# Optimization experiments

Hardware: AMD Instinct MI355X
Metric: run time of the kernel (lower is better)

Reference implementation:

```python
import jax, jax.numpy as jnp
import numpy as np

N, MAX_NB, H, L, V, B, M = 16384, 15, 512, 128, 1024, 256, 65536


def setup_inputs() -> dict:
    key = jax.random.key(0)
    ks = jax.random.split(key, 32)
    s = 0.02  # param init scale
    inp = {
        'x_ids': jax.random.randint(ks[0], (N,), 0, V, dtype=jnp.int32),
        'contexts': jax.random.randint(ks[1], (N,), 0, B, dtype=jnp.int32),
        'nei_idx': jax.random.randint(ks[2], (N, MAX_NB), 0, M, dtype=jnp.int32),
        'nei_mask': jax.random.randint(ks[3], (N, MAX_NB), 0, 2, dtype=jnp.int32),
        'o_idx': jax.random.randint(ks[4], (N, MAX_NB), 0, M, dtype=jnp.int32),
        'o_mask': jax.random.randint(ks[5], (N, MAX_NB), 0, 2, dtype=jnp.int32),
        'H_msg': jax.random.normal(ks[6], (M, H), jnp.float32),
        'x_tree_vecs': jax.random.normal(ks[7], (B, L), jnp.float32),
        'embedding': jax.random.normal(ks[8], (V, H), jnp.float32) * s,
        'Wz_w': jax.random.normal(ks[9], (H, 2 * H), jnp.float32) * s,
        'Wz_b': jnp.zeros((H,), jnp.float32),
        'Wr_w': jax.random.normal(ks[10], (H, H), jnp.float32) * s,
        'Wr_b': jnp.zeros((H,), jnp.float32),
        'Ur_w': jax.random.normal(ks[11], (H, H), jnp.float32) * s,
        'Wh_w': jax.random.normal(ks[12], (H, 2 * H), jnp.float32) * s,
        'Wh_b': jnp.zeros((H,), jnp.float32),
        'W_w': jax.random.normal(ks[13], (H, H + L), jnp.float32) * s,
        'W_b': jnp.zeros((H,), jnp.float32),
        'Wo_w': jax.random.normal(ks[14], (V, H), jnp.float32) * s,
        'Wo_b': jnp.zeros((V,), jnp.float32),
        'Ui_w': jax.random.normal(ks[15], (H, 2 * H), jnp.float32) * s,
        'Ui_b': jnp.zeros((H,), jnp.float32),
        'U_w': jax.random.normal(ks[16], (H, H + L), jnp.float32) * s,
        'U_b': jnp.zeros((H,), jnp.float32),
        'Uo_w': jax.random.normal(ks[17], (1, H), jnp.float32) * s,
        'Uo_b': jnp.zeros((1,), jnp.float32),
    }
    return inp


def _gru(x, h_nei, Wz_w, Wz_b, Wr_w, Wr_b, Ur_w, Wh_w, Wh_b):
    # x: [N,H], h_nei: [N,MAX_NB,H]
    sum_h = h_nei.sum(axis=1)
    z = jax.nn.sigmoid(jnp.concatenate([x, sum_h], axis=1) @ Wz_w.T + Wz_b)
    r1 = (x @ Wr_w.T + Wr_b)[:, None, :]          # [N,1,H]
    r2 = jnp.einsum('nkh,gh->nkg', h_nei, Ur_w)   # U_r(h_nei), no bias
    r = jax.nn.sigmoid(r1 + r2)
    sum_gated = (r * h_nei).sum(axis=1)
    pre_h = jnp.tanh(jnp.concatenate([x, sum_gated], axis=1) @ Wh_w.T + Wh_b)
    return (1.0 - z) * sum_h + z * pre_h


def reference(x_ids, contexts, nei_idx, nei_mask, o_idx, o_mask, H_msg,
              x_tree_vecs, embedding, Wz_w, Wz_b, Wr_w, Wr_b, Ur_w,
              Wh_w, Wh_b, W_w, W_b, Wo_w, Wo_b, Ui_w, Ui_b, U_w, U_b,
              Uo_w, Uo_b):
    x = embedding[x_ids]                                   # [N,H]
    h_nei = H_msg[nei_idx] * nei_mask[..., None].astype(H_msg.dtype)  # [N,NB,H]
    o_nei = H_msg[o_idx] * o_mask[..., None].astype(H_msg.dtype)
    new_h = _gru(x, h_nei, Wz_w, Wz_b, Wr_w, Wr_b, Ur_w, Wh_w, Wh_b)
    cur_o = o_nei.sum(axis=1)                              # [N,H]
    ctx = x_tree_vecs[contexts]                            # [N,L]
    # word prediction: aggregate(new_h, contexts, x_tree_vecs, 'word')
    w_hid = jax.nn.relu(jnp.concatenate([new_h, ctx], axis=1) @ W_w.T + W_b)
    word_scores = w_hid @ Wo_w.T + Wo_b                    # [N,V]
    # stop prediction: U_i(cat(x, cur_o)) -> aggregate(..., 'stop')
    stop_h = jax.nn.relu(jnp.concatenate([x, cur_o], axis=1) @ Ui_w.T + Ui_b)
    s_hid = jax.nn.relu(jnp.concatenate([stop_h, ctx], axis=1) @ U_w.T + U_b)
    stop_scores = s_hid @ Uo_w.T + Uo_b                    # [N,1]
    return jnp.concatenate([word_scores, stop_scores], axis=1)  # [N,V+1]
```

## Files before the change

### kernel.cpp

```cpp
#include <hip/hip_runtime.h>
#include <hip/hip_bf16.h>

typedef unsigned short u16;
typedef unsigned int u32;
typedef __attribute__((ext_vector_type(8))) short s8v;
typedef __attribute__((ext_vector_type(4))) float f4v;

#define HDIM 512
#define NNODE 16384
#define NB 15

__device__ __forceinline__ u16 f2bu(float x) {
  union { float f; u32 i; } v; v.f = x;
  u32 r = v.i + 0x7FFFu + ((v.i >> 16) & 1u);
  return (u16)(r >> 16);
}
__device__ __forceinline__ float bu2f(u16 u) {
  union { u32 i; float f; } v; v.i = ((u32)u) << 16;
  return v.f;
}
__device__ __forceinline__ u32 pk(float a, float b) {
  return (u32)f2bu(a) | ((u32)f2bu(b) << 16);
}
__device__ __forceinline__ float sigm(float x) {
  return __builtin_amdgcn_rcpf(1.f + __expf(-x));
}
__device__ __forceinline__ void gl16(const void* g, void* l) {
  __builtin_amdgcn_global_load_lds(
      (const __attribute__((address_space(1))) u32*)g,
      (__attribute__((address_space(3))) u32*)l, 16, 0, 0);
}
template<int N> __device__ __forceinline__ void wait_vm() {
  if constexpr (N == 0) asm volatile("s_waitcnt vmcnt(0)" ::: "memory");
  else if constexpr (N == 2) asm volatile("s_waitcnt vmcnt(2)" ::: "memory");
  else asm volatile("s_waitcnt vmcnt(4)" ::: "memory");
}

__global__ __launch_bounds__(256) void k_cvt_all(
    const float* Wz_w, const float* Wr_w, const float* Wh_w, const float* Ui_w,
    const float* Ur_w, const float* W_w, const float* U_w, const float* Wo_w,
    const float* emb, const float* xtree,
    const float* Wz_b, const float* Wr_b, const float* Wh_b, const float* Ui_b,
    const float* W_b, const float* U_b,
    u16* wcat, u16* wz_h, u16* wh_h, u16* ui_h, u16* ur, u16* w_n, u16* u_n,
    u16* ccat, u16* wo, u16* emb_bf, u16* xt_bf, float* ebias, float* cbias) {
  int seg = blockIdx.y;
  const float* src = nullptr; u16* dst = nullptr;
  const float* fsrc = nullptr; float* fdst = nullptr;
  int R = 0, Cs = 0, c0 = 0, C = 0, fn = 0;
  switch (seg) {
    case 0:  src = Wz_w; dst = wcat;              R = 512;  Cs = 1024; c0 = 0;   C = 512; break;
    case 1:  src = Wr_w; dst = wcat + 512 * 512;  R = 512;  Cs = 512;  c0 = 0;   C = 512; break;
    case 2:  src = Wh_w; dst = wcat + 1024 * 512; R = 512;  Cs = 1024; c0 = 0;   C = 512; break;
    case 3:  src = Ui_w; dst = wcat + 1536 * 512; R = 512;  Cs = 1024; c0 = 0;   C = 512; break;
    case 4:  src = Wz_w; dst = wz_h;              R = 512;  Cs = 1024; c0 = 512; C = 512; break;
    case 5:  src = Wh_w; dst = wh_h;              R = 512;  Cs = 1024; c0 = 512; C = 512; break;
    case 6:  src = Ui_w; dst = ui_h;              R = 512;  Cs = 1024; c0 = 512; C = 512; break;
    case 7:  src = Ur_w; dst = ur;                R = 512;  Cs = 512;  c0 = 0;   C = 512; break;
    case 8:  src = W_w;  dst = w_n;               R = 512;  Cs = 640;  c0 = 0;   C = 512; break;
    case 9:  src = U_w;  dst = u_n;               R = 512;  Cs = 640;  c0 = 0;   C = 512; break;
    case 10: src = W_w;  dst = ccat;              R = 512;  Cs = 640;  c0 = 512; C = 128; break;
    case 11: src = U_w;  dst = ccat + 512 * 128;  R = 512;  Cs = 640;  c0 = 512; C = 128; break;
    case 12: src = Wo_w; dst = wo;                R = 1024; Cs = 512;  c0 = 0;   C = 512; break;
    case 13: src = emb;  dst = emb_bf;            R = 1024; Cs = 512;  c0 = 0;   C = 512; break;
    case 14: src = xtree; dst = xt_bf;            R = 256;  Cs = 128;  c0 = 0;   C = 128; break;
    case 15: fsrc = Wz_b; fdst = ebias;        fn = 512; break;
    case 16: fsrc = Wr_b; fdst = ebias + 512;  fn = 512; break;
    case 17: fsrc = Wh_b; fdst = ebias + 1024; fn = 512; break;
    case 18: fsrc = Ui_b; fdst = ebias + 1536; fn = 512; break;
    case 19: fsrc = W_b;  fdst = cbias;        fn = 512; break;
    case 20: fsrc = U_b;  fdst = cbias + 512;  fn = 512; break;
  }
  int i = blockIdx.x * 256 + threadIdx.x;
  if (fdst) { if (i < fn) fdst[i] = fsrc[i]; return; }
  int e0 = i * 8;
  if (e0 >= R * C) return;
  int r = e0 / C, c = e0 - r * C;
  const float* s = src + (size_t)r * Cs + c0 + c;
  float4 a = *reinterpret_cast<const float4*>(s);
  float4 b = *reinterpret_cast<const float4*>(s + 4);
  uint4 o = {pk(a.x, a.y), pk(a.z, a.w), pk(b.x, b.y), pk(b.z, b.w)};
  *reinterpret_cast<uint4*>(&dst[e0]) = o;
}

struct GP {
  const u16* A; const u16* B; int K; int lda;
  const float* gadd; int ldg; const int* gidx;
  const float* bias; const u16* shb;
  float* outf; u16* outh; int ldo;
};

template<int EP>
__device__ __forceinline__ void epi(int row, int col, float v, const GP& g) {
  if constexpr (EP == 0) {
    g.outf[(size_t)row * g.ldo + col] = v + (g.bias ? g.bias[col] : 0.f);
  } else if constexpr (EP == 3) {
    float pre = v + g.gadd[(size_t)g.gidx[row] * g.ldg + col];
    g.outh[(size_t)row * g.ldo + col] = f2bu(pre > 0.f ? pre : 0.f);
  } else {
    g.outh[(size_t)row * g.ldo + col] = f2bu(v);
  }
}

__device__ __forceinline__ void swz_tile(int nx, int ny, int& m0, int& n0) {
  int orig = blockIdx.y * nx + blockIdx.x;
  int q = (nx * ny) >> 3;
  int tile = (orig & 7) * q + (orig >> 3);
  n0 = (tile % nx) * 128;
  m0 = (tile / nx) * 128;
}

template<int EP, int KV>
__device__ void gemm_core(const GP& g, u16* AsB, u16* BsB, int m0, int n0) {
  const int tid = threadIdx.x, lane = tid & 63, w = tid >> 6;
  const int wm = (w >> 2) * 64, wn = (w & 3) * 32;

  const int sr = tid >> 2, sc = (tid & 3) ^ ((sr >> 1) & 3);
  const u16* gA = g.A + (size_t)(m0 + sr) * g.lda + sc * 8;
  const u16* gB = g.B + (size_t)(n0 + sr) * KV + sc * 8;
  const int ls = tid * 8;

  f4v acc[4][2];
  f4v z4 = {0.f, 0.f, 0.f, 0.f};
#pragma unroll
  for (int a = 0; a < 4; a++) { acc[a][0] = z4; acc[a][1] = z4; }

  constexpr int T = KV / 32;
  auto STAGE = [&](int t) {
    int buf = (t & 3) * 4096;
    gl16(gA + t * 32, AsB + buf + ls);
    gl16(gB + t * 32, BsB + buf + ls);
  };
  STAGE(0); STAGE(1); STAGE(2);

#pragma unroll
  for (int t = 0; t < T; t++) {
    if (t < T - 2) wait_vm<4>();
    else if (t == T - 2) wait_vm<2>();
    else wait_vm<0>();
    __builtin_amdgcn_s_barrier();
    asm volatile("" ::: "memory");
    if (t + 3 < T) STAGE(t + 3);
    const u16* as = AsB + (t & 3) * 4096;
    const u16* bs = BsB + (t & 3) * 4096;
    s8v af[4], bf[2];
    int cc = lane >> 4;
#pragma unroll
    for (int i = 0; i < 4; i++) {
      int R = wm + i * 16 + (lane & 15);
      af[i] = *reinterpret_cast<const s8v*>(
          &as[R * 32 + (cc ^ ((R >> 1) & 3)) * 8]);
    }
#pragma unroll
    for (int i = 0; i < 2; i++) {
      int C = wn + i * 16 + (lane & 15);
      bf[i] = *reinterpret_cast<const s8v*>(
          &bs[C * 32 + (cc ^ ((C >> 1) & 3)) * 8]);
    }
    __builtin_amdgcn_s_setprio(1);
#pragma unroll
    for (int mi = 0; mi < 4; mi++)
#pragma unroll
      for (int ni = 0; ni < 2; ni++)
        acc[mi][ni] = __builtin_amdgcn_mfma_f32_16x16x32_bf16(
            af[mi], bf[ni], acc[mi][ni], 0, 0, 0);
    __builtin_amdgcn_s_setprio(0);
  }
#pragma unroll
  for (int mi = 0; mi < 4; mi++)
#pragma unroll
    for (int ni = 0; ni < 2; ni++)
#pragma unroll
      for (int r = 0; r < 4; r++) {
        int row = m0 + wm + mi * 16 + (lane >> 4) * 4 + r;
        int col = n0 + wn + ni * 16 + (lane & 15);
        epi<EP>(row, col, acc[mi][ni][r], g);
      }
}

template<int EP, int KV>
__device__ void gemm_2buf(const GP& g, u16* AsB, u16* BsB, int m0, int n0) {
  const int tid = threadIdx.x, lane = tid & 63, w = tid >> 6;
  const int wm = (w >> 2) * 64, wn = (w & 3) * 32;
  const int sr = tid >> 2, sc = (tid & 3) ^ ((sr >> 1) & 3);
  const u16* gA = g.A + (size_t)(m0 + sr) * g.lda + sc * 8;
  const u16* gB = g.B + (size_t)(n0 + sr) * KV + sc * 8;
  const int ls = tid * 8;

  f4v acc[4][2];
  f4v z4 = {0.f, 0.f, 0.f, 0.f};
#pragma unroll
  for (int a = 0; a < 4; a++) { acc[a][0] = z4; acc[a][1] = z4; }

  constexpr int T = KV / 32;
  auto STAGE = [&](int t) {
    int buf = (t & 1) * 4096;
    gl16(gA + t * 32, AsB + buf + ls);
    gl16(gB + t * 32, BsB + buf + ls);
  };
  STAGE(0);
#pragma unroll
  for (int t = 0; t < T; t++) {
    __syncthreads();
    if (t + 1 < T) STAGE(t + 1);
    const u16* as = AsB + (t & 1) * 4096;
    const u16* bs = BsB + (t & 1) * 4096;
    s8v af[4], bf[2];
    int cc = lane >> 4;
#pragma unroll
    for (int i = 0; i < 4; i++) {
      int R = wm + i * 16 + (lane & 15);
      af[i] = *reinterpret_cast<const s8v*>(
          &as[R * 32 + (cc ^ ((R >> 1) & 3)) * 8]);
    }
#pragma unroll
    for (int i = 0; i < 2; i++) {
      int C = wn + i * 16 + (lane & 15);
      bf[i] = *reinterpret_cast<const s8v*>(
          &bs[C * 32 + (cc ^ ((C >> 1) & 3)) * 8]);
    }
    __builtin_amdgcn_s_setprio(1);
#pragma unroll
    for (int mi = 0; mi < 4; mi++)
#pragma unroll
      for (int ni = 0; ni < 2; ni++)
        acc[mi][ni] = __builtin_amdgcn_mfma_f32_16x16x32_bf16(
            af[mi], bf[ni], acc[mi][ni], 0, 0, 0);
    __builtin_amdgcn_s_setprio(0);
  }
#pragma unroll
  for (int mi = 0; mi < 4; mi++)
#pragma unroll
    for (int ni = 0; ni < 2; ni++)
#pragma unroll
      for (int r = 0; r < 4; r++) {
        int row = m0 + wm + mi * 16 + (lane >> 4) * 4 + r;
        int col = n0 + wn + ni * 16 + (lane & 15);
        epi<EP>(row, col, acc[mi][ni][r], g);
      }
}

template<int EP, int KV>
__global__ __launch_bounds__(512, 4) void k_gemm(GP g) {
  __shared__ u16 As[4 * 4096], Bs[4 * 4096];
  int m0, n0;
  swz_tile(gridDim.x, gridDim.y, m0, n0);
  gemm_core<EP, KV>(g, As, Bs, m0, n0);
}

template<int EPa, int EPb, int KV>
__global__ __launch_bounds__(512, 4) void k_pair(GP a, GP b) {
  __shared__ u16 As[4 * 4096], Bs[4 * 4096];
  int m0, n0;
  swz_tile(gridDim.x, gridDim.y, m0, n0);
  if (blockIdx.z == 0) gemm_core<EPa, KV>(a, As, Bs, m0, n0);
  else gemm_core<EPb, KV>(b, As, Bs, m0, n0);
}

__global__ __launch_bounds__(512, 4) void k_mix(
    const float* __restrict__ src, u16* __restrict__ Hb, GP ge, GP gc) {
  __shared__ u16 S[16384];
  int id = blockIdx.x;
  if (id < 128) {
    gemm_2buf<0, 512>(ge, S, S + 8192, (id >> 4) * 128, (id & 15) * 128);
    return;
  }
  if (id < 144) {
    int t = id - 128;
    gemm_2buf<0, 128>(gc, S, S + 8192, (t >> 3) * 128, (t & 7) * 128);
    return;
  }
  size_t i = ((size_t)(id - 144) * 512 + threadIdx.x) * 8;
  float4 a = *reinterpret_cast<const float4*>(src + i);
  float4 b = *reinterpret_cast<const float4*>(src + i + 4);
  uint4 o = {pk(a.x, a.y), pk(a.z, a.w), pk(b.x, b.y), pk(b.z, b.w)};
  *reinterpret_cast<uint4*>(&Hb[i]) = o;
}

__global__ __launch_bounds__(512, 4) void k_znp(
    const u16* __restrict__ sumh, const u16* __restrict__ sg,
    const u16* __restrict__ Wz, const u16* __restrict__ Wh,
    const float* __restrict__ E_z, const float* __restrict__ E_h, int ldg,
    const int* __restrict__ gidx, u16* __restrict__ newh, GP gs) {
  __shared__ u16 S[32768];
  int m0, n0;
  swz_tile(gridDim.x, gridDim.y, m0, n0);
  if (blockIdx.z == 1) { gemm_core<3, 512>(gs, S, S + 16384, m0, n0); return; }
  const int tid = threadIdx.x, lane = tid & 63, w = tid >> 6;
  const int wm = (w >> 2) * 64, wn = (w & 3) * 32;

  const int sr = tid >> 2, sc = (tid & 3) ^ ((sr >> 1) & 3);
  const u16* gA[2] = {sumh + (size_t)(m0 + sr) * HDIM + sc * 8,
                      sg + (size_t)(m0 + sr) * HDIM + sc * 8};
  const u16* gB[2] = {Wz + (size_t)(n0 + sr) * HDIM + sc * 8,
                      Wh + (size_t)(n0 + sr) * HDIM + sc * 8};
  const int ls = tid * 8;
  u16* AsB = S;
  u16* BsB = S + 16384;
  auto STAGE = [&](int s) {
    int p = s & 1, k0 = (s >> 1) * 32;
    int buf = (s & 3) * 4096;
    gl16(gA[p] + k0, AsB + buf + ls);
    gl16(gB[p] + k0, BsB + buf + ls);
  };

  f4v az[4][2], ah[4][2];
  f4v z4 = {0.f, 0.f, 0.f, 0.f};
#pragma unroll
  for (int a = 0; a < 4; a++) {
    az[a][0] = z4; az[a][1] = z4; ah[a][0] = z4; ah[a][1] = z4;
  }

  STAGE(0); STAGE(1); STAGE(2);
#pragma unroll
  for (int s = 0; s < 32; s++) {
    if (s < 30) wait_vm<4>();
    else if (s == 30) wait_vm<2>();
    else wait_vm<0>();
    __builtin_amdgcn_s_barrier();
    asm volatile("" ::: "memory");
    if (s + 3 < 32) STAGE(s + 3);
    const u16* as = AsB + (s & 3) * 4096;
    const u16* bs = BsB + (s & 3) * 4096;
    s8v af[4], bf[2];
    int cc = lane >> 4;
#pragma unroll
    for (int i = 0; i < 4; i++) {
      int R = wm + i * 16 + (lane & 15);
      af[i] = *reinterpret_cast<const s8v*>(
          &as[R * 32 + (cc ^ ((R >> 1) & 3)) * 8]);
    }
#pragma unroll
    for (int i = 0; i < 2; i++) {
      int C = wn + i * 16 + (lane & 15);
      bf[i] = *reinterpret_cast<const s8v*>(
          &bs[C * 32 + (cc ^ ((C >> 1) & 3)) * 8]);
    }
    f4v (&acc)[4][2] = (s & 1) ? ah : az;
    __builtin_amdgcn_s_setprio(1);
#pragma unroll
    for (int mi = 0; mi < 4; mi++)
#pragma unroll
      for (int ni = 0; ni < 2; ni++)
        acc[mi][ni] = __builtin_amdgcn_mfma_f32_16x16x32_bf16(
            af[mi], bf[ni], acc[mi][ni], 0, 0, 0);
    __builtin_amdgcn_s_setprio(0);
  }
#pragma unroll
  for (int mi = 0; mi < 4; mi++)
#pragma unroll
    for (int r = 0; r < 4; r++) {
      int row = m0 + wm + mi * 16 + (lane >> 4) * 4 + r;
      int xid = gidx[row];
      const float* ez = E_z + (size_t)xid * ldg;
      const float* eh = E_h + (size_t)xid * ldg;
#pragma unroll
      for (int ni = 0; ni < 2; ni++) {
        int col = n0 + wn + ni * 16 + (lane & 15);
        float zv = sigm(az[mi][ni][r] + ez[col]);
        float pre = tanhf(ah[mi][ni][r] + eh[col]);
        float sh = bu2f(sumh[(size_t)row * HDIM + col]);
        newh[(size_t)row * HDIM + col] = f2bu((1.f - zv) * sh + zv * pre);
      }
    }
}

__global__ __launch_bounds__(256) void k_gsr(
    const u16* __restrict__ Hb, const u16* __restrict__ R2,
    const float* __restrict__ E_r, int ldg, const int* __restrict__ x_ids,
    const int* __restrict__ nei_idx, const int* __restrict__ nei_mask,
    const int* __restrict__ o_idx, const int* __restrict__ o_mask,
    u16* __restrict__ sum_h_bf, u16* __restrict__ sg_bf,
    u16* __restrict__ cur_o_bf) {
  int t = threadIdx.x;
  int nd = t >> 6, lane = t & 63;
  int n = blockIdx.x * 4 + nd;
  __shared__ int sidx[4][NB], smsk[4][NB], soid[4][NB], somk[4][NB];
  __shared__ int sx[4];
  if (t < 60) {
    int nn = t / 15, k = t - nn * 15;
    size_t gofs = (size_t)(blockIdx.x * 4 + nn) * NB + k;
    sidx[nn][k] = nei_idx[gofs];
    smsk[nn][k] = nei_mask[gofs];
  } else if (t >= 64 && t < 124) {
    int tt = t - 64;
    int nn = tt / 15, k = tt - nn * 15;
    size_t gofs = (size_t)(blockIdx.x * 4 + nn) * NB + k;
    soid[nn][k] = o_idx[gofs];
    somk[nn][k] = o_mask[gofs];
  } else if (t >= 128 && t < 132) {
    sx[t - 128] = x_ids[blockIdx.x * 4 + (t - 128)];
  }
  __syncthreads();
  int c = lane * 8;
  const float* er = E_r + (size_t)sx[nd] * ldg + c;
  float4 e0 = *reinterpret_cast<const float4*>(er);
  float4 e1 = *reinterpret_cast<const float4*>(er + 4);
  float ev[8] = {e0.x, e0.y, e0.z, e0.w, e1.x, e1.y, e1.z, e1.w};
  float s[8], gg[8], oo[8];
#pragma unroll
  for (int i = 0; i < 8; i++) { s[i] = 0.f; gg[i] = 0.f; oo[i] = 0.f; }
#pragma unroll
  for (int k = 0; k < NB; k++) {
    if (smsk[nd][k]) {
      size_t rb = (size_t)sidx[nd][k] * HDIM + c;
      uint4 hv = *reinterpret_cast<const uint4*>(Hb + rb);
      uint4 rv = *reinterpret_cast<const uint4*>(R2 + rb);
      u32 ha[4] = {hv.x, hv.y, hv.z, hv.w};
      u32 ra[4] = {rv.x, rv.y, rv.z, rv.w};
#pragma unroll
      for (int p = 0; p < 4; p++) {
        float h0 = bu2f((u16)ha[p]), h1 = bu2f((u16)(ha[p] >> 16));
        s[p * 2] += h0; s[p * 2 + 1] += h1;
        gg[p * 2] += sigm(bu2f((u16)ra[p]) + ev[p * 2]) * h0;
        gg[p * 2 + 1] += sigm(bu2f((u16)(ra[p] >> 16)) + ev[p * 2 + 1]) * h1;
      }
    }
    if (somk[nd][k]) {
      uint4 ov = *reinterpret_cast<const uint4*>(
          Hb + (size_t)soid[nd][k] * HDIM + c);
      u32 oa[4] = {ov.x, ov.y, ov.z, ov.w};
#pragma unroll
      for (int p = 0; p < 4; p++) {
        oo[p * 2] += bu2f((u16)oa[p]);
        oo[p * 2 + 1] += bu2f((u16)(oa[p] >> 16));
      }
    }
  }
  size_t b = (size_t)n * HDIM + c;
  uint4 ps = {pk(s[0], s[1]), pk(s[2], s[3]), pk(s[4], s[5]), pk(s[6], s[7])};
  uint4 pg = {pk(gg[0], gg[1]), pk(gg[2], gg[3]), pk(gg[4], gg[5]), pk(gg[6], gg[7])};
  uint4 po = {pk(oo[0], oo[1]), pk(oo[2], oo[3]), pk(oo[4], oo[5]), pk(oo[6], oo[7])};
  *reinterpret_cast<uint4*>(&sum_h_bf[b]) = ps;
  *reinterpret_cast<uint4*>(&sg_bf[b]) = pg;
  *reinterpret_cast<uint4*>(&cur_o_bf[b]) = po;
}

__global__ __launch_bounds__(512, 4) void k_wordstop(
    GP wgp, const u16* __restrict__ shid, const float* __restrict__ Uo_w,
    const float* __restrict__ Uo_b, float* __restrict__ out) {
  __shared__ u16 As[4 * 4096], Bs[4 * 4096];
  if (blockIdx.z == 0) {
    int m0, n0;
    swz_tile(gridDim.x, gridDim.y, m0, n0);
    gemm_core<0, 512>(wgp, As, Bs, m0, n0);
    return;
  }
  int b = blockIdx.y * gridDim.x + blockIdx.x;
  int wv = threadIdx.x >> 6, lane = threadIdx.x & 63;
#pragma unroll
  for (int i = 0; i < 2; i++) {
    int n = b * 16 + wv * 2 + i;
    const u16* row = shid + (size_t)n * HDIM + lane * 8;
    const float* uw = Uo_w + lane * 8;
    uint4 v = *reinterpret_cast<const uint4*>(row);
    float4 u0 = *reinterpret_cast<const float4*>(uw);
    float4 u1 = *reinterpret_cast<const float4*>(uw + 4);
    float s = bu2f((u16)v.x) * u0.x + bu2f((u16)(v.x >> 16)) * u0.y +
              bu2f((u16)v.y) * u0.z + bu2f((u16)(v.y >> 16)) * u0.w +
              bu2f((u16)v.z) * u1.x + bu2f((u16)(v.z >> 16)) * u1.y +
              bu2f((u16)v.w) * u1.z + bu2f((u16)(v.w >> 16)) * u1.w;
#pragma unroll
    for (int off = 32; off; off >>= 1) s += __shfl_xor(s, off, 64);
    if (lane == 0) out[(size_t)n * 1025 + 1024] = s + Uo_b[0];
  }
}

extern "C" void kernel_launch(void* const* d_in, const int* in_sizes, int n_in,
                              void* d_out, int out_size, void* d_ws, size_t ws_size,
                              hipStream_t stream) {
  const int* x_ids = (const int*)d_in[0];
  const int* contexts = (const int*)d_in[1];
  const int* nei_idx = (const int*)d_in[2];
  const int* nei_mask = (const int*)d_in[3];
  const int* o_idx = (const int*)d_in[4];
  const int* o_mask = (const int*)d_in[5];
  const float* H_msg = (const float*)d_in[6];
  const float* xtree = (const float*)d_in[7];
  const float* emb = (const float*)d_in[8];
  const float* Wz_w = (const float*)d_in[9];  const float* Wz_b = (const float*)d_in[10];
  const float* Wr_w = (const float*)d_in[11]; const float* Wr_b = (const float*)d_in[12];
  const float* Ur_w = (const float*)d_in[13];
  const float* Wh_w = (const float*)d_in[14]; const float* Wh_b = (const float*)d_in[15];
  const float* W_w  = (const float*)d_in[16]; const float* W_b  = (const float*)d_in[17];
  const float* Wo_w = (const float*)d_in[18]; const float* Wo_b = (const float*)d_in[19];
  const float* Ui_w = (const float*)d_in[20]; const float* Ui_b = (const float*)d_in[21];
  const float* U_w  = (const float*)d_in[22]; const float* U_b  = (const float*)d_in[23];
  const float* Uo_w = (const float*)d_in[24]; const float* Uo_b = (const float*)d_in[25];
  float* out = (float*)d_out;
  const int M = 65536;

  char* base = (char*)d_ws;
  size_t ofs = 0;
  auto alloc = [&](size_t bytes) -> char* {
    char* p = base + ofs;
    ofs = (ofs + bytes + 255) & ~(size_t)255;
    return p;
  };
  u16* wcat  = (u16*)alloc((size_t)2048 * 512 * 2);
  u16* wz_h  = (u16*)alloc(512 * 512 * 2);
  u16* wh_h  = (u16*)alloc(512 * 512 * 2);
  u16* ui_h  = (u16*)alloc(512 * 512 * 2);
  u16* ur    = (u16*)alloc(512 * 512 * 2);
  u16* w_n   = (u16*)alloc(512 * 512 * 2);
  u16* u_n   = (u16*)alloc(512 * 512 * 2);
  u16* ccat  = (u16*)alloc(1024 * 128 * 2);
  u16* wo    = (u16*)alloc(1024 * 512 * 2);
  u16* emb_bf = (u16*)alloc(1024 * 512 * 2);
  u16* xt_bf  = (u16*)alloc(256 * 128 * 2);
  float* ebias = (float*)alloc(2048 * 4);
  float* cbias = (float*)alloc(1024 * 4);
  float* E_cat = (float*)alloc((size_t)1024 * 2048 * 4);
  float* C_cat = (float*)alloc((size_t)256 * 1024 * 4);
  u16* H_bf = (u16*)alloc((size_t)M * HDIM * 2);
  u16* R2   = (u16*)alloc((size_t)M * HDIM * 2);
  u16* sum_h_bf = (u16*)alloc((size_t)NNODE * HDIM * 2);
  u16* cur_o_bf = (u16*)alloc((size_t)NNODE * HDIM * 2);
  u16* sg_bf    = (u16*)alloc((size_t)NNODE * HDIM * 2);
  u16* newh_bf  = (u16*)alloc((size_t)NNODE * HDIM * 2);
  u16* whid_bf  = (u16*)alloc((size_t)NNODE * HDIM * 2);
  u16* stoph_bf = (u16*)alloc((size_t)NNODE * HDIM * 2);
  u16* shid_bf  = (u16*)alloc((size_t)NNODE * HDIM * 2);

  k_cvt_all<<<dim3(256, 21), dim3(256), 0, stream>>>(
      Wz_w, Wr_w, Wh_w, Ui_w, Ur_w, W_w, U_w, Wo_w, emb, xtree,
      Wz_b, Wr_b, Wh_b, Ui_b, W_b, U_b,
      wcat, wz_h, wh_h, ui_h, ur, w_n, u_n, ccat, wo, emb_bf, xt_bf,
      ebias, cbias);

  GP ge{emb_bf, wcat, 512, 512, nullptr, 0, nullptr, ebias, nullptr,
        E_cat, nullptr, 2048};
  GP gc{xt_bf, ccat, 128, 128, nullptr, 0, nullptr, cbias, nullptr,
        C_cat, nullptr, 1024};
  k_mix<<<dim3(8336), dim3(512), 0, stream>>>(H_msg, H_bf, ge, gc);

  GP gr{H_bf, ur, 512, 512, nullptr, 0, nullptr, nullptr, nullptr,
        nullptr, R2, 512};
  k_gemm<4, 512><<<dim3(4, 512), dim3(512), 0, stream>>>(gr);

  k_gsr<<<dim3(NNODE / 4), dim3(256), 0, stream>>>(
      H_bf, R2, E_cat + 512, 2048, x_ids, nei_idx, nei_mask, o_idx, o_mask,
      sum_h_bf, sg_bf, cur_o_bf);

  GP gs{cur_o_bf, ui_h, 512, 512, E_cat + 1536, 2048, x_ids, nullptr, nullptr,
        nullptr, stoph_bf, 512};
  k_znp<<<dim3(4, 128, 2), dim3(512), 0, stream>>>(
      sum_h_bf, sg_bf, wz_h, wh_h, E_cat, E_cat + 1024, 2048, x_ids,
      newh_bf, gs);

  GP gw{newh_bf, w_n, 512, 512, C_cat, 1024, contexts, nullptr, nullptr,
        nullptr, whid_bf, 512};
  GP gu{stoph_bf, u_n, 512, 512, C_cat + 512, 1024, contexts, nullptr, nullptr,
        nullptr, shid_bf, 512};
  k_pair<3, 3, 512><<<dim3(4, 128, 2), dim3(512), 0, stream>>>(gw, gu);

  GP gword{whid_bf, wo, 512, 512, nullptr, 0, nullptr, Wo_b, nullptr,
           out, nullptr, 1025};
  k_wordstop<<<dim3(8, 128, 2), dim3(512), 0, stream>>>(
      gword, shid_bf, Uo_w, Uo_b, out);
}
```

Before: 294.3 us.

## Fuse H_msg bf16 conversion into the Ur GEMM that reads it

The standalone fp32-to-bf16 conversion of H_msg and the separate R2 = H·Urᵀ GEMM kernel are merged into one kernel. Each GEMM block loads fp32 rows of H_msg, packs them to bf16 in registers, stores them to shared memory for the MFMA loop, and the n0==0 blocks also write the bf16 copy back for later gathers. This drops one kernel launch and a full bf16 round trip of H_msg through memory. The cost is that the A operand is now loaded synchronously through registers with double buffering, rather than by the async path, and fp32 reads are repeated across the four column blocks.

```diff
diff --git a/kernel.cpp b/kernel.cpp
--- a/kernel.cpp
+++ b/kernel.cpp
@@ -240,14 +240,6 @@
       }
 }
 
-template<int EP, int KV>
-__global__ __launch_bounds__(512, 4) void k_gemm(GP g) {
-  __shared__ u16 As[4 * 4096], Bs[4 * 4096];
-  int m0, n0;
-  swz_tile(gridDim.x, gridDim.y, m0, n0);
-  gemm_core<EP, KV>(g, As, Bs, m0, n0);
-}
-
 template<int EPa, int EPb, int KV>
 __global__ __launch_bounds__(512, 4) void k_pair(GP a, GP b) {
   __shared__ u16 As[4 * 4096], Bs[4 * 4096];
@@ -257,8 +249,9 @@
   else gemm_core<EPb, KV>(b, As, Bs, m0, n0);
 }
 
-__global__ __launch_bounds__(512, 4) void k_mix(
-    const float* __restrict__ src, u16* __restrict__ Hb, GP ge, GP gc) {
+__global__ __launch_bounds__(512, 4) void k_mixR(
+    const float* __restrict__ Hf, u16* __restrict__ Hb, u16* __restrict__ R2,
+    const u16* __restrict__ ur, GP ge, GP gc) {
   __shared__ u16 S[16384];
   int id = blockIdx.x;
   if (id < 128) {
@@ -270,11 +263,85 @@
     gemm_2buf<0, 128>(gc, S, S + 8192, (t >> 3) * 128, (t & 7) * 128);
     return;
   }
-  size_t i = ((size_t)(id - 144) * 512 + threadIdx.x) * 8;
-  float4 a = *reinterpret_cast<const float4*>(src + i);
-  float4 b = *reinterpret_cast<const float4*>(src + i + 4);
-  uint4 o = {pk(a.x, a.y), pk(a.z, a.w), pk(b.x, b.y), pk(b.z, b.w)};
-  *reinterpret_cast<uint4*>(&Hb[i]) = o;
+  const int rid = id - 144;
+  const int m0 = (rid >> 2) * 128, n0 = (rid & 3) * 128;
+  const int tid = threadIdx.x, lane = tid & 63, w = tid >> 6;
+  const int wm = (w >> 2) * 64, wn = (w & 3) * 32;
+  const int sr = tid >> 2;
+  const int c4 = tid & 3;
+  const int scB = c4 ^ ((sr >> 1) & 3);
+  const float* gAf = Hf + (size_t)(m0 + sr) * HDIM + c4 * 8;
+  const u16* gB = ur + (size_t)(n0 + sr) * HDIM + scB * 8;
+  u16* hOut = (n0 == 0) ? Hb + (size_t)(m0 + sr) * HDIM + c4 * 8 : nullptr;
+  u16* AsB = S;
+  u16* BsB = S + 8192;
+  const int lsB = tid * 8;
+  const int lsA = sr * 32 + (c4 ^ ((sr >> 1) & 3)) * 8;
+
+  f4v acc[4][2];
+  f4v z4 = {0.f, 0.f, 0.f, 0.f};
+#pragma unroll
+  for (int a = 0; a < 4; a++) { acc[a][0] = z4; acc[a][1] = z4; }
+
+  {
+    float4 a0 = *reinterpret_cast<const float4*>(gAf);
+    float4 a1 = *reinterpret_cast<const float4*>(gAf + 4);
+    gl16(gB, BsB + lsB);
+    uint4 v = {pk(a0.x, a0.y), pk(a0.z, a0.w), pk(a1.x, a1.y), pk(a1.z, a1.w)};
+    *reinterpret_cast<uint4*>(&AsB[lsA]) = v;
+    if (hOut) *reinterpret_cast<uint4*>(hOut) = v;
+  }
+  __syncthreads();
+#pragma unroll
+  for (int t = 0; t < 16; t++) {
+    float4 na0, na1;
+    if (t + 1 < 16) {
+      na0 = *reinterpret_cast<const float4*>(gAf + (t + 1) * 32);
+      na1 = *reinterpret_cast<const float4*>(gAf + (t + 1) * 32 + 4);
+      gl16(gB + (t + 1) * 32, BsB + ((t + 1) & 1) * 4096 + lsB);
+    }
+    const u16* as = AsB + (t & 1) * 4096;
+    const u16* bs = BsB + (t & 1) * 4096;
+    s8v af[4], bf[2];
+    int cc = lane >> 4;
+#pragma unroll
+    for (int i = 0; i < 4; i++) {
+      int R = wm + i * 16 + (lane & 15);
+      af[i] = *reinterpret_cast<const s8v*>(
+          &as[R * 32 + (cc ^ ((R >> 1) & 3)) * 8]);
+    }
+#pragma unroll
+    for (int i = 0; i < 2; i++) {
+      int C = wn + i * 16 + (lane & 15);
+      bf[i] = *reinterpret_cast<const s8v*>(
+          &bs[C * 32 + (cc ^ ((C >> 1) & 3)) * 8]);
+    }
+    __builtin_amdgcn_s_setprio(1);
+#pragma unroll
+    for (int mi = 0; mi < 4; mi++)
+#pragma unroll
+      for (int ni = 0; ni < 2; ni++)
+        acc[mi][ni] = __builtin_amdgcn_mfma_f32_16x16x32_bf16(
+            af[mi], bf[ni], acc[mi][ni], 0, 0, 0);
+    __builtin_amdgcn_s_setprio(0);
+    if (t + 1 < 16) {
+      uint4 v = {pk(na0.x, na0.y), pk(na0.z, na0.w),
+                 pk(na1.x, na1.y), pk(na1.z, na1.w)};
+      *reinterpret_cast<uint4*>(&AsB[((t + 1) & 1) * 4096 + lsA]) = v;
+      if (hOut) *reinterpret_cast<uint4*>(hOut + (size_t)(t + 1) * 32) = v;
+      __syncthreads();
+    }
+  }
+#pragma unroll
+  for (int mi = 0; mi < 4; mi++)
+#pragma unroll
+    for (int ni = 0; ni < 2; ni++)
+#pragma unroll
+      for (int r = 0; r < 4; r++) {
+        int row = m0 + wm + mi * 16 + (lane >> 4) * 4 + r;
+        int col = n0 + wn + ni * 16 + (lane & 15);
+        R2[(size_t)row * HDIM + col] = f2bu(acc[mi][ni][r]);
+      }
 }
 
 __global__ __launch_bounds__(512, 4) void k_znp(
@@ -532,11 +599,8 @@
         E_cat, nullptr, 2048};
   GP gc{xt_bf, ccat, 128, 128, nullptr, 0, nullptr, cbias, nullptr,
         C_cat, nullptr, 1024};
-  k_mix<<<dim3(8336), dim3(512), 0, stream>>>(H_msg, H_bf, ge, gc);
-
-  GP gr{H_bf, ur, 512, 512, nullptr, 0, nullptr, nullptr, nullptr,
-        nullptr, R2, 512};
-  k_gemm<4, 512><<<dim3(4, 512), dim3(512), 0, stream>>>(gr);
+  k_mixR<<<dim3(144 + 2048), dim3(512), 0, stream>>>(
+      H_msg, H_bf, R2, ur, ge, gc);
 
   k_gsr<<<dim3(NNODE / 4), dim3(256), 0, stream>>>(
       H_bf, R2, E_cat + 512, 2048, x_ids, nei_idx, nei_mask, o_idx, o_mask,
```

Result: slower. 332.8 us (+13.1%).
